# Kernel optimization log

Measured on AMD Instinct MI355X. Metric: run time of the kernel, lower is better.

The kernel has to match this reference:

```python
import jax, jax.numpy as jnp
import numpy as np

PAST = 15        # sum(num_classes[:-1])
NC = 20          # sum(num_classes)
ALPHA = 0.99
IGNORE = 255


def setup_inputs() -> dict:
    key = jax.random.key(0)
    k1, k2, k3, k4, k5, k6 = jax.random.split(key, 6)
    B, C, H, W = 8, NC, 512, 512
    logit = jax.random.normal(k1, (B, C, H, W), dtype=jnp.float32)
    # ema_prob is used as probabilities (gathered & compared to thresholds)
    ema_prob = jax.nn.softmax(jax.random.normal(k2, (B, C, H, W), dtype=jnp.float32), axis=1)
    ema_thresh = jax.random.uniform(k3, (NC,), dtype=jnp.float32, minval=0.2, maxval=0.8)
    real_labels = jax.random.randint(k4, (B, H, W), 0, NC, dtype=jnp.int64)
    # sprinkle ignore pixels (255) like real segmentation masks
    real_labels = jnp.where(jax.random.uniform(k5, (B, H, W)) < 0.1, IGNORE, real_labels)
    moving_prob_avg = jax.random.uniform(k6, (NC,), dtype=jnp.float32)
    return {"logit": logit, "ema_prob": ema_prob, "ema_thresh": ema_thresh,
            "real_labels": real_labels, "moving_prob_avg": moving_prob_avg}


def reference(logit, ema_prob, ema_thresh, real_labels, moving_prob_avg):
    # --- pseudo-labels from current model (detached softmax) ---
    logit_prob = jax.nn.softmax(jax.lax.stop_gradient(logit), axis=1)  # [B,C,H,W]
    labels = jnp.argmax(logit_prob[:, :PAST], axis=1)                   # [B,H,W]
    labels = jnp.where(real_labels >= PAST, real_labels, labels)
    idx = jnp.where(real_labels == IGNORE, 0, labels)
    scores = jnp.take_along_axis(logit_prob, idx[:, None], axis=1)[:, 0]  # [B,H,W]

    # --- per-class mean of scores + EMA update of moving_prob_avg ---
    flat_lab = labels.reshape(-1)
    flat_sc = scores.reshape(-1)
    seg = jnp.where(flat_lab == IGNORE, NC, flat_lab)  # route ignored to extra bucket
    sums = jax.ops.segment_sum(flat_sc, seg, num_segments=NC + 1)[:NC]
    counts = jax.ops.segment_sum(jnp.ones_like(flat_sc), seg, num_segments=NC + 1)[:NC]
    means = sums / jnp.maximum(counts, 1.0)
    mpa = moving_prob_avg  # numpy buffer in torch (no grad)
    new_mpa = jnp.where(counts > 0,
                        jnp.where(mpa == -1.0, means, (1.0 - ALPHA) * means + ALPHA * mpa),
                        mpa)

    # --- EMA-teacher pseudo labels + threshold mask ---
    ema_labels = jnp.argmax(ema_prob[:, :PAST], axis=1)
    ema_labels = jnp.where(real_labels >= PAST, real_labels, ema_labels)
    eidx = jnp.where(real_labels == IGNORE, 0, ema_labels)
    ema_scores = jnp.take_along_axis(ema_prob, eidx[:, None], axis=1)[:, 0]
    valid_cls = ema_labels < NC  # 255 never matches any class in the torch loop
    thr = ema_thresh[jnp.clip(ema_labels, 0, NC - 1)]
    ema_mask = valid_cls & (ema_scores >= thr)
    dynamic_labels = jnp.where(ema_mask, ema_labels, IGNORE)  # [B,H,W]

    # --- masked cross-entropy with per-class reweighting ---
    logp = jax.nn.log_softmax(logit, axis=1)
    cidx = jnp.clip(dynamic_labels, 0, NC - 1)
    losses = -jnp.take_along_axis(logp, cidx[:, None], axis=1)[:, 0]
    valid = dynamic_labels != IGNORE
    mult = jnp.where(valid, 1.0 - new_mpa[cidx], 1.0)
    losses = losses * jax.lax.stop_gradient(mult)  # multiplier is a host scalar in torch
    vs = valid.astype(losses.dtype)
    return jnp.sum(losses * vs) / jnp.sum(vs)
```

## Files before the change

### kernel.cpp

```cpp
#include <hip/hip_runtime.h>
#include <math.h>


#define PASTC 15
#define NCC   20
#define IGN   255
#define HW2   262144
#define ALPHAF 0.99f

__global__ __launch_bounds__(256) void dl_main(
    const float* __restrict__ logit,
    const float* __restrict__ ema,
    const float* __restrict__ thresh,
    const int*   __restrict__ real,
    float*       __restrict__ ws)
{
    __shared__ float s_acc[61];
    const int tid = threadIdx.x;
    if (tid < 61) s_acc[tid] = 0.0f;
    __syncthreads();

    const int t  = blockIdx.x * 256 + tid;
    const int p0 = t << 2;
    const int b  = p0 >> 18;
    const int s  = p0 & (HW2 - 1);
    const size_t base = (((size_t)(b * NCC)) << 18) + (size_t)s;

    const int4 rl4 = *reinterpret_cast<const int4*>(real + p0);
    const int rl[4] = {rl4.x, rl4.y, rl4.z, rl4.w};

    int   cap_ch[4];
    float e_m15[4], e_cap[4];
    int   e_arg[4];
#pragma unroll
    for (int j = 0; j < 4; ++j) {
        cap_ch[j] = (rl[j] == IGN) ? 0 : (rl[j] >= PASTC ? rl[j] : -1);
        e_m15[j]  = -INFINITY;
        e_cap[j]  = 0.0f;
        e_arg[j]  = 0;
    }

#pragma unroll
    for (int c = 0; c < NCC; ++c) {
        const float4 v = *reinterpret_cast<const float4*>(ema + base + ((size_t)c << 18));
        const float vv[4] = {v.x, v.y, v.z, v.w};
#pragma unroll
        for (int j = 0; j < 4; ++j) {
            if (c < PASTC && vv[j] > e_m15[j]) { e_m15[j] = vv[j]; e_arg[j] = c; }
            if (c == cap_ch[j]) e_cap[j] = vv[j];
        }
    }

    int cidx[4];
#pragma unroll
    for (int j = 0; j < 4; ++j) {
        const int   el  = (rl[j] >= PASTC) ? rl[j] : e_arg[j];
        const float esc = (cap_ch[j] >= 0) ? e_cap[j] : e_m15[j];
        const float th  = thresh[el < NCC ? el : (NCC - 1)];
        const bool  valid = (el < NCC) && (esc >= th);
        cidx[j] = valid ? el : -1;
    }

    float m20[4], se[4], m15[4], capS[4], capL[4];
    int   arg15[4];
#pragma unroll
    for (int j = 0; j < 4; ++j) {
        m20[j] = -INFINITY; se[j] = 0.0f; m15[j] = -INFINITY;
        capS[j] = 0.0f; capL[j] = 0.0f; arg15[j] = 0;
    }

#pragma unroll
    for (int c = 0; c < NCC; ++c) {
        const float4 v = *reinterpret_cast<const float4*>(logit + base + ((size_t)c << 18));
        const float vv[4] = {v.x, v.y, v.z, v.w};
#pragma unroll
        for (int j = 0; j < 4; ++j) {
            const float x  = vv[j];
            const float mo = m20[j];
            const float e  = __expf(-fabsf(x - mo));
            const bool  g  = x > mo;
            se[j]  = g ? fmaf(se[j], e, 1.0f) : (se[j] + e);
            m20[j] = fmaxf(mo, x);
            if (c < PASTC && x > m15[j]) { m15[j] = x; arg15[j] = c; }
            if (c == cap_ch[j]) capS[j] = x;
            if (c == cidx[j])   capL[j] = x;
        }
    }

#pragma unroll
    for (int j = 0; j < 4; ++j) {
        const float lse = m20[j] + __logf(se[j]);
        if (rl[j] != IGN) {
            const int   lab  = (rl[j] >= PASTC) ? rl[j] : arg15[j];
            const float sval = (cap_ch[j] >= 0) ? capS[j] : m15[j];
            const float prob = __expf(sval - lse);
            atomicAdd(&s_acc[lab], prob);
            atomicAdd(&s_acc[20 + lab], 1.0f);
        }
        if (cidx[j] >= 0) {
            atomicAdd(&s_acc[40 + cidx[j]], lse - capL[j]);
        }
        const unsigned long long bm = __ballot(cidx[j] >= 0);
        if ((tid & 63) == 0) atomicAdd(&s_acc[60], (float)__popcll(bm));
    }

    __syncthreads();
    if (tid < 61) atomicAdd(&ws[tid], s_acc[tid]);
}

__global__ void dl_final(const float* __restrict__ ws,
                         const float* __restrict__ mpa,
                         float*       __restrict__ out)
{
    if (threadIdx.x == 0 && blockIdx.x == 0) {
        float acc = 0.0f;
        for (int c = 0; c < NCC; ++c) {
            const float ssum = ws[c];
            const float cnt  = ws[20 + c];
            const float lsum = ws[40 + c];
            const float m    = mpa[c];
            const float mean = ssum / fmaxf(cnt, 1.0f);
            const float nm   = (cnt > 0.0f)
                                 ? ((m == -1.0f) ? mean
                                                 : (1.0f - ALPHAF) * mean + ALPHAF * m)
                                 : m;
            acc += lsum * (1.0f - nm);
        }
        out[0] = acc / ws[60];
    }
}

extern "C" void kernel_launch(void* const* d_in, const int* in_sizes, int n_in,
                              void* d_out, int out_size, void* d_ws, size_t ws_size,
                              hipStream_t stream) {
    const float* logit  = (const float*)d_in[0];
    const float* ema    = (const float*)d_in[1];
    const float* thresh = (const float*)d_in[2];
    const int*   real   = (const int*)d_in[3];
    const float* mpa    = (const float*)d_in[4];
    float* out = (float*)d_out;
    float* ws  = (float*)d_ws;

    hipMemsetAsync(ws, 0, 64 * sizeof(float), stream);

    dl_main<<<2048, 256, 0, stream>>>(logit, ema, thresh, real, ws);
    dl_final<<<1, 64, 0, stream>>>(ws, mpa, out);
}
```

Measured before the change: 353.5 us.

## Halve per-thread pixels, batch channel loads upfront, fuse finalize via last-block counter

```diff
diff --git a/kernel.cpp b/kernel.cpp
--- a/kernel.cpp
+++ b/kernel.cpp
@@ -13,7 +13,9 @@
     const float* __restrict__ ema,
     const float* __restrict__ thresh,
     const int*   __restrict__ real,
-    float*       __restrict__ ws)
+    const float* __restrict__ mpa,
+    float*       __restrict__ ws,
+    float*       __restrict__ out)
 {
     __shared__ float s_acc[61];
     const int tid = threadIdx.x;
@@ -21,39 +23,40 @@
     __syncthreads();
 
     const int t  = blockIdx.x * 256 + tid;
-    const int p0 = t << 2;
+    const int p0 = t << 1;
     const int b  = p0 >> 18;
     const int s  = p0 & (HW2 - 1);
     const size_t base = (((size_t)(b * NCC)) << 18) + (size_t)s;
 
-    const int4 rl4 = *reinterpret_cast<const int4*>(real + p0);
-    const int rl[4] = {rl4.x, rl4.y, rl4.z, rl4.w};
+    const int2 rl2 = *reinterpret_cast<const int2*>(real + p0);
+    const int rl[2] = {rl2.x, rl2.y};
 
-    int   cap_ch[4];
-    float e_m15[4], e_cap[4];
-    int   e_arg[4];
+    int cap_ch[2];
 #pragma unroll
-    for (int j = 0; j < 4; ++j) {
+    for (int j = 0; j < 2; ++j)
         cap_ch[j] = (rl[j] == IGN) ? 0 : (rl[j] >= PASTC ? rl[j] : -1);
-        e_m15[j]  = -INFINITY;
-        e_cap[j]  = 0.0f;
-        e_arg[j]  = 0;
-    }
 
+    float2 ev[NCC];
+#pragma unroll
+    for (int c = 0; c < NCC; ++c)
+        ev[c] = *reinterpret_cast<const float2*>(ema + base + ((size_t)c << 18));
+
+    float e_m15[2] = {-INFINITY, -INFINITY};
+    float e_cap[2] = {0.0f, 0.0f};
+    int   e_arg[2] = {0, 0};
 #pragma unroll
     for (int c = 0; c < NCC; ++c) {
-        const float4 v = *reinterpret_cast<const float4*>(ema + base + ((size_t)c << 18));
-        const float vv[4] = {v.x, v.y, v.z, v.w};
+        const float vv[2] = {ev[c].x, ev[c].y};
 #pragma unroll
-        for (int j = 0; j < 4; ++j) {
+        for (int j = 0; j < 2; ++j) {
             if (c < PASTC && vv[j] > e_m15[j]) { e_m15[j] = vv[j]; e_arg[j] = c; }
             if (c == cap_ch[j]) e_cap[j] = vv[j];
         }
     }
 
-    int cidx[4];
+    int cidx[2];
 #pragma unroll
-    for (int j = 0; j < 4; ++j) {
+    for (int j = 0; j < 2; ++j) {
         const int   el  = (rl[j] >= PASTC) ? rl[j] : e_arg[j];
         const float esc = (cap_ch[j] >= 0) ? e_cap[j] : e_m15[j];
         const float th  = thresh[el < NCC ? el : (NCC - 1)];
@@ -61,20 +64,23 @@
         cidx[j] = valid ? el : -1;
     }
 
-    float m20[4], se[4], m15[4], capS[4], capL[4];
-    int   arg15[4];
+    float2 lv[NCC];
 #pragma unroll
-    for (int j = 0; j < 4; ++j) {
-        m20[j] = -INFINITY; se[j] = 0.0f; m15[j] = -INFINITY;
-        capS[j] = 0.0f; capL[j] = 0.0f; arg15[j] = 0;
-    }
+    for (int c = 0; c < NCC; ++c)
+        lv[c] = *reinterpret_cast<const float2*>(logit + base + ((size_t)c << 18));
+
+    float m20[2]  = {-INFINITY, -INFINITY};
+    float se[2]   = {0.0f, 0.0f};
+    float m15[2]  = {-INFINITY, -INFINITY};
+    float capS[2] = {0.0f, 0.0f};
+    float capL[2] = {0.0f, 0.0f};
+    int   arg15[2] = {0, 0};
 
 #pragma unroll
     for (int c = 0; c < NCC; ++c) {
-        const float4 v = *reinterpret_cast<const float4*>(logit + base + ((size_t)c << 18));
-        const float vv[4] = {v.x, v.y, v.z, v.w};
+        const float vv[2] = {lv[c].x, lv[c].y};
 #pragma unroll
-        for (int j = 0; j < 4; ++j) {
+        for (int j = 0; j < 2; ++j) {
             const float x  = vv[j];
             const float mo = m20[j];
             const float e  = __expf(-fabsf(x - mo));
@@ -88,7 +94,7 @@
     }
 
 #pragma unroll
-    for (int j = 0; j < 4; ++j) {
+    for (int j = 0; j < 2; ++j) {
         const float lse = m20[j] + __logf(se[j]);
         if (rl[j] != IGN) {
             const int   lab  = (rl[j] >= PASTC) ? rl[j] : arg15[j];
@@ -106,27 +112,28 @@
 
     __syncthreads();
     if (tid < 61) atomicAdd(&ws[tid], s_acc[tid]);
-}
 
-__global__ void dl_final(const float* __restrict__ ws,
-                         const float* __restrict__ mpa,
-                         float*       __restrict__ out)
-{
-    if (threadIdx.x == 0 && blockIdx.x == 0) {
-        float acc = 0.0f;
-        for (int c = 0; c < NCC; ++c) {
-            const float ssum = ws[c];
-            const float cnt  = ws[20 + c];
-            const float lsum = ws[40 + c];
-            const float m    = mpa[c];
-            const float mean = ssum / fmaxf(cnt, 1.0f);
-            const float nm   = (cnt > 0.0f)
-                                 ? ((m == -1.0f) ? mean
-                                                 : (1.0f - ALPHAF) * mean + ALPHAF * m)
-                                 : m;
-            acc += lsum * (1.0f - nm);
+    __threadfence();
+    __syncthreads();
+    if (tid == 0) {
+        unsigned* ctr = reinterpret_cast<unsigned*>(ws) + 61;
+        const unsigned prev = atomicAdd(ctr, 1u);
+        if (prev == gridDim.x - 1) {
+            float acc = 0.0f;
+            for (int c = 0; c < NCC; ++c) {
+                const float ssum = atomicAdd(&ws[c], 0.0f);
+                const float cnt  = atomicAdd(&ws[20 + c], 0.0f);
+                const float lsum = atomicAdd(&ws[40 + c], 0.0f);
+                const float m    = mpa[c];
+                const float mean = ssum / fmaxf(cnt, 1.0f);
+                const float nm   = (cnt > 0.0f)
+                                     ? ((m == -1.0f) ? mean
+                                                     : (1.0f - ALPHAF) * mean + ALPHAF * m)
+                                     : m;
+                acc += lsum * (1.0f - nm);
+            }
+            out[0] = acc / atomicAdd(&ws[60], 0.0f);
         }
-        out[0] = acc / ws[60];
     }
 }
 
@@ -143,6 +150,5 @@
 
     hipMemsetAsync(ws, 0, 64 * sizeof(float), stream);
 
-    dl_main<<<2048, 256, 0, stream>>>(logit, ema, thresh, real, ws);
-    dl_final<<<1, 64, 0, stream>>>(ws, mpa, out);
+    dl_main<<<4096, 256, 0, stream>>>(logit, ema, thresh, real, mpa, ws, out);
 }
```

After: 998.5 us. +182.4%, slower.

## Process one pixel per thread with interleaved, software-prefetched ema/logit channel loads

Applied to the files above, without the earlier changes.

```diff
diff --git a/kernel.cpp b/kernel.cpp
--- a/kernel.cpp
+++ b/kernel.cpp
@@ -8,7 +8,7 @@
 #define HW2   262144
 #define ALPHAF 0.99f
 
-__global__ __launch_bounds__(256) void dl_main(
+__global__ __launch_bounds__(256, 8) void dl_main(
     const float* __restrict__ logit,
     const float* __restrict__ ema,
     const float* __restrict__ thresh,
@@ -20,89 +20,77 @@
     if (tid < 61) s_acc[tid] = 0.0f;
     __syncthreads();
 
-    const int t  = blockIdx.x * 256 + tid;
-    const int p0 = t << 2;
-    const int b  = p0 >> 18;
-    const int s  = p0 & (HW2 - 1);
+    const int t = blockIdx.x * 256 + tid;
+    const int b = t >> 18;
+    const int s = t & (HW2 - 1);
     const size_t base = (((size_t)(b * NCC)) << 18) + (size_t)s;
 
-    const int4 rl4 = *reinterpret_cast<const int4*>(real + p0);
-    const int rl[4] = {rl4.x, rl4.y, rl4.z, rl4.w};
+    const int rl = real[t];
+    const int cap_ch = (rl == IGN) ? 0 : (rl >= PASTC ? rl : -1);
 
-    int   cap_ch[4];
-    float e_m15[4], e_cap[4];
-    int   e_arg[4];
+    float e_m15 = -INFINITY, e_cap = 0.0f;
+    int   e_arg = 0;
+    float m20 = -INFINITY, se = 0.0f, m15 = -INFINITY, capS = 0.0f;
+    int   arg15 = 0;
+
+    float ecur[5], lcur[5];
 #pragma unroll
-    for (int j = 0; j < 4; ++j) {
-        cap_ch[j] = (rl[j] == IGN) ? 0 : (rl[j] >= PASTC ? rl[j] : -1);
-        e_m15[j]  = -INFINITY;
-        e_cap[j]  = 0.0f;
-        e_arg[j]  = 0;
+    for (int i = 0; i < 5; ++i) {
+        ecur[i] = ema  [base + ((size_t)i << 18)];
+        lcur[i] = logit[base + ((size_t)i << 18)];
     }
 
 #pragma unroll
-    for (int c = 0; c < NCC; ++c) {
-        const float4 v = *reinterpret_cast<const float4*>(ema + base + ((size_t)c << 18));
-        const float vv[4] = {v.x, v.y, v.z, v.w};
+    for (int g = 0; g < 4; ++g) {
+        float enxt[5], lnxt[5];
+        if (g < 3) {
 #pragma unroll
-        for (int j = 0; j < 4; ++j) {
-            if (c < PASTC && vv[j] > e_m15[j]) { e_m15[j] = vv[j]; e_arg[j] = c; }
-            if (c == cap_ch[j]) e_cap[j] = vv[j];
+            for (int i = 0; i < 5; ++i) {
+                enxt[i] = ema  [base + ((size_t)(g * 5 + 5 + i) << 18)];
+                lnxt[i] = logit[base + ((size_t)(g * 5 + 5 + i) << 18)];
+            }
+        }
+#pragma unroll
+        for (int i = 0; i < 5; ++i) {
+            const int   c = g * 5 + i;
+            const float e = ecur[i];
+            const float x = lcur[i];
+            if (c < PASTC && e > e_m15) { e_m15 = e; e_arg = c; }
+            if (c == cap_ch) e_cap = e;
+            const float mo = m20;
+            const float ex = __expf(-fabsf(x - mo));
+            se  = (x > mo) ? fmaf(se, ex, 1.0f) : (se + ex);
+            m20 = fmaxf(mo, x);
+            if (c < PASTC && x > m15) { m15 = x; arg15 = c; }
+            if (c == cap_ch) capS = x;
+        }
+        if (g < 3) {
+#pragma unroll
+            for (int i = 0; i < 5; ++i) { ecur[i] = enxt[i]; lcur[i] = lnxt[i]; }
         }
     }
 
-    int cidx[4];
-#pragma unroll
-    for (int j = 0; j < 4; ++j) {
-        const int   el  = (rl[j] >= PASTC) ? rl[j] : e_arg[j];
-        const float esc = (cap_ch[j] >= 0) ? e_cap[j] : e_m15[j];
-        const float th  = thresh[el < NCC ? el : (NCC - 1)];
-        const bool  valid = (el < NCC) && (esc >= th);
-        cidx[j] = valid ? el : -1;
+    const int   el    = (rl >= PASTC) ? rl : e_arg;
+    const float esc   = (cap_ch >= 0) ? e_cap : e_m15;
+    const float th    = thresh[el < NCC ? el : (NCC - 1)];
+    const bool  valid = (el < NCC) && (esc >= th);
+    const int   cidx  = valid ? el : -1;
+
+    const float lse = m20 + __logf(se);
+
+    if (rl != IGN) {
+        const int   lab  = (rl >= PASTC) ? rl : arg15;
+        const float sval = (cap_ch >= 0) ? capS : m15;
+        const float prob = __expf(sval - lse);
+        atomicAdd(&s_acc[lab], prob);
+        atomicAdd(&s_acc[20 + lab], 1.0f);
     }
-
-    float m20[4], se[4], m15[4], capS[4], capL[4];
-    int   arg15[4];
-#pragma unroll
-    for (int j = 0; j < 4; ++j) {
-        m20[j] = -INFINITY; se[j] = 0.0f; m15[j] = -INFINITY;
-        capS[j] = 0.0f; capL[j] = 0.0f; arg15[j] = 0;
+    if (cidx >= 0) {
+        const float capL = logit[base + ((size_t)cidx << 18)];
+        atomicAdd(&s_acc[40 + cidx], lse - capL);
     }
-
-#pragma unroll
-    for (int c = 0; c < NCC; ++c) {
-        const float4 v = *reinterpret_cast<const float4*>(logit + base + ((size_t)c << 18));
-        const float vv[4] = {v.x, v.y, v.z, v.w};
-#pragma unroll
-        for (int j = 0; j < 4; ++j) {
-            const float x  = vv[j];
-            const float mo = m20[j];
-            const float e  = __expf(-fabsf(x - mo));
-            const bool  g  = x > mo;
-            se[j]  = g ? fmaf(se[j], e, 1.0f) : (se[j] + e);
-            m20[j] = fmaxf(mo, x);
-            if (c < PASTC && x > m15[j]) { m15[j] = x; arg15[j] = c; }
-            if (c == cap_ch[j]) capS[j] = x;
-            if (c == cidx[j])   capL[j] = x;
-        }
-    }
-
-#pragma unroll
-    for (int j = 0; j < 4; ++j) {
-        const float lse = m20[j] + __logf(se[j]);
-        if (rl[j] != IGN) {
-            const int   lab  = (rl[j] >= PASTC) ? rl[j] : arg15[j];
-            const float sval = (cap_ch[j] >= 0) ? capS[j] : m15[j];
-            const float prob = __expf(sval - lse);
-            atomicAdd(&s_acc[lab], prob);
-            atomicAdd(&s_acc[20 + lab], 1.0f);
-        }
-        if (cidx[j] >= 0) {
-            atomicAdd(&s_acc[40 + cidx[j]], lse - capL[j]);
-        }
-        const unsigned long long bm = __ballot(cidx[j] >= 0);
-        if ((tid & 63) == 0) atomicAdd(&s_acc[60], (float)__popcll(bm));
-    }
+    const unsigned long long bm = __ballot(cidx >= 0);
+    if ((tid & 63) == 0) atomicAdd(&s_acc[60], (float)__popcll(bm));
 
     __syncthreads();
     if (tid < 61) atomicAdd(&ws[tid], s_acc[tid]);
@@ -143,6 +131,6 @@
 
     hipMemsetAsync(ws, 0, 64 * sizeof(float), stream);
 
-    dl_main<<<2048, 256, 0, stream>>>(logit, ema, thresh, real, ws);
+    dl_main<<<8192, 256, 0, stream>>>(logit, ema, thresh, real, ws);
     dl_final<<<1, 64, 0, stream>>>(ws, mpa, out);
 }
```

Result: slower. 450.5 us (+27.4%).
